# Performance work log

Measured on AMD Instinct MI355X. Metric: run time of the kernel, lower is better.

The kernel has to match this reference:

```python
import jax, jax.numpy as jnp
import numpy as np

EPS = 1e-8  # matches torch F.cosine_similarity eps


def setup_inputs() -> dict:
    key = jax.random.key(0)
    S, U, D = 2048, 10, 256  # speakers, utterances/speaker, embedding dim
    embeddings = jax.random.normal(key, (S * U, D), dtype=jnp.float32)
    labels = jnp.repeat(jnp.arange(S, dtype=jnp.int64), U)  # speaker-blocked, as the view() assumes
    return {"embeddings": embeddings, "labels": labels}


def reference(embeddings, labels):
    labels_np = np.asarray(labels)
    S = int(np.unique(labels_np).size)          # num_speakers (static)
    B, D = embeddings.shape
    U = B // S                                   # num_utterances
    E = embeddings.reshape(S, U, D)
    C = E.mean(axis=1)                           # (S, D) centroids
    En = E / jnp.maximum(jnp.linalg.norm(E, axis=-1, keepdims=True), EPS)
    Cn = C / jnp.maximum(jnp.linalg.norm(C, axis=-1, keepdims=True), EPS)
    sim = jnp.einsum('sud,kd->suk', En, Cn)      # (S, U, S) cosine similarities
    idx = jnp.arange(S)
    pos = sim[idx, :, idx]                       # (S, U) similarity to own centroid
    neg_mask = jnp.eye(S, dtype=bool)[:, None, :]  # mask out k == i
    neg = jnp.where(neg_mask, -jnp.inf, sim)
    lse = jax.nn.logsumexp(neg, axis=-1)         # (S, U)
    loss = jnp.mean(-pos + lse)
    return loss
```

## Files before the change

kernel.cpp:

```cpp
#include <hip/hip_runtime.h>
#include <math.h>

#define SS   2048
#define UU   10
#define DD   256
#define BB   (SS * UU)
#define EPSF 1e-8f

typedef __attribute__((ext_vector_type(8))) short   bf16x8;
typedef __attribute__((ext_vector_type(4))) float   floatx4;

__device__ static inline unsigned short f2bf(float f) {
    union { float f; unsigned u; } v; v.f = f;
    unsigned r = (v.u + 0x7FFFu + ((v.u >> 16) & 1u)) >> 16;
    return (unsigned short)r;
}

__device__ static inline void gl_lds16(const unsigned short* g, unsigned short* l) {
    __builtin_amdgcn_global_load_lds((const __attribute__((address_space(1))) void*)g,
                                     (__attribute__((address_space(3))) void*)l, 16, 0, 0);
}

__global__ __launch_bounds__(256) void prep_kernel(const float* __restrict__ E,
                                                   unsigned short* __restrict__ Enb,
                                                   unsigned short* __restrict__ Cnb,
                                                   float* __restrict__ sumexp,
                                                   float* __restrict__ out) {
    const int wid = threadIdx.x >> 6, lane = threadIdx.x & 63;

    if (threadIdx.x < 80) sumexp[blockIdx.x * 80 + threadIdx.x] = 0.f;
    if (blockIdx.x == 0 && threadIdx.x == 0) out[0] = 0.f;

#pragma unroll
    for (int sp2 = 0; sp2 < 2; ++sp2) {
        const int sp = blockIdx.x * 8 + wid * 2 + sp2;
        const float* rb = E + (size_t)sp * UU * DD + lane * 4;

        float4 v[UU];
#pragma unroll
        for (int u = 0; u < UU; ++u) v[u] = *(const float4*)(rb + u * DD);

        float ssq[UU];
#pragma unroll
        for (int u = 0; u < UU; ++u)
            ssq[u] = v[u].x * v[u].x + v[u].y * v[u].y + v[u].z * v[u].z + v[u].w * v[u].w;
#pragma unroll
        for (int off = 32; off; off >>= 1) {
#pragma unroll
            for (int u = 0; u < UU; ++u) ssq[u] += __shfl_xor(ssq[u], off, 64);
        }

        unsigned short* eb = Enb + (size_t)sp * UU * DD + lane * 4;
        float cx = 0.f, cy = 0.f, cz = 0.f, cw = 0.f;
#pragma unroll
        for (int u = 0; u < UU; ++u) {
            const float rinv = 1.0f / fmaxf(sqrtf(ssq[u]), EPSF);
            ushort4 o;
            o.x = f2bf(v[u].x * rinv); o.y = f2bf(v[u].y * rinv);
            o.z = f2bf(v[u].z * rinv); o.w = f2bf(v[u].w * rinv);
            *(ushort4*)(eb + u * DD) = o;
            cx += v[u].x; cy += v[u].y; cz += v[u].z; cw += v[u].w;
        }

        cx *= 0.1f; cy *= 0.1f; cz *= 0.1f; cw *= 0.1f;
        float cs = cx * cx + cy * cy + cz * cz + cw * cw;
#pragma unroll
        for (int off = 32; off; off >>= 1) cs += __shfl_xor(cs, off, 64);
        const float rinv = 1.0f / fmaxf(sqrtf(cs), EPSF);
        ushort4 oc;
        oc.x = f2bf(cx * rinv); oc.y = f2bf(cy * rinv);
        oc.z = f2bf(cz * rinv); oc.w = f2bf(cw * rinv);
        *(ushort4*)(Cnb + (size_t)sp * DD + lane * 4) = oc;
    }
}

#define BM  128
#define BN  128
#define BK  32
#define NBN 2

__device__ __forceinline__ void chunk_mfma(const unsigned short* Ab,
                                           const unsigned short* Bb,
                                           const int* aoff, const int* boff,
                                           floatx4 (&acc)[4][4]) {
    bf16x8 af[4], bfr[4];
#pragma unroll
    for (int t = 0; t < 4; ++t) af[t]  = *(const bf16x8*)(Ab + aoff[t]);
#pragma unroll
    for (int t = 0; t < 4; ++t) bfr[t] = *(const bf16x8*)(Bb + boff[t]);
#pragma unroll
    for (int mt = 0; mt < 4; ++mt)
#pragma unroll
        for (int nt = 0; nt < 4; ++nt)
            acc[mt][nt] = __builtin_amdgcn_mfma_f32_16x16x32_bf16(af[mt], bfr[nt], acc[mt][nt], 0, 0, 0);
}

__global__ __launch_bounds__(256) void gemm_lse_kernel(const unsigned short* __restrict__ Enb,
                                                       const unsigned short* __restrict__ Cnb,
                                                       float* __restrict__ posArr,
                                                       float* __restrict__ sumexp) {
    __shared__ unsigned short As[BM * BK];
    __shared__ unsigned short Bs[BN * BK];

    const int tid  = threadIdx.x;
    const int wid  = tid >> 6, lane = tid & 63;
    const int l15  = lane & 15, quad = lane >> 4;
    const int wave_m = wid >> 1, wave_n = wid & 1;

    const int swz = (blockIdx.x & 7) * 160 + (blockIdx.x >> 3);
    const int bm  = swz >> 3;
    const int bnb = (swz & 7) * NBN;
    const int row0 = bm * BM;

    const int rl = lane >> 2;
    const int gf = ((lane & 3) ^ ((rl >> 1) & 3)) * 8;
    const unsigned short* gpA[4];
    unsigned short* lp[4];
    size_t goffB[4];
#pragma unroll
    for (int i = 0; i < 4; ++i) {
        const int c = wid * 4 + i;
        if (c < 8) {
            gpA[i]  = Enb + (size_t)(row0 + c * 16 + rl) * DD + gf;
            lp[i]   = As + c * 512;
            goffB[i] = 0;
        } else {
            gpA[i]  = nullptr;
            lp[i]   = Bs + (c - 8) * 512;
            goffB[i] = (size_t)((c - 8) * 16 + rl) * DD + gf;
        }
    }

    const int fswz = (quad ^ ((l15 >> 1) & 3)) * 8;
    int aoff[4], boff[4];
#pragma unroll
    for (int t = 0; t < 4; ++t) {
        aoff[t] = (wave_m * 64 + t * 16 + l15) * BK + fswz;
        boff[t] = (wave_n * 64 + t * 16 + l15) * BK + fswz;
    }

    int lbl[4][4];
    float rs[4][4];
#pragma unroll
    for (int mt = 0; mt < 4; ++mt) {
        const int growb = row0 + wave_m * 64 + mt * 16 + quad * 4;
#pragma unroll
        for (int r = 0; r < 4; ++r) {
            lbl[mt][r] = (growb + r) / UU;
            rs[mt][r]  = 0.f;
        }
    }

    floatx4 acc[4][4];

#pragma unroll
    for (int bl = 0; bl < NBN; ++bl) {
        const int n0 = (bnb + bl) * BN;
        const unsigned short* gp[4];
#pragma unroll
        for (int i = 0; i < 4; ++i) {
            const int c = wid * 4 + i;
            gp[i] = (c < 8) ? gpA[i] : (Cnb + (size_t)n0 * DD + goffB[i]);
        }

#pragma unroll
        for (int i = 0; i < 4; ++i)
#pragma unroll
            for (int j = 0; j < 4; ++j) acc[i][j] = (floatx4){0.f, 0.f, 0.f, 0.f};

        for (int k0 = 0; k0 < DD; k0 += BK) {
            __syncthreads();
#pragma unroll
            for (int i = 0; i < 4; ++i) gl_lds16(gp[i] + k0, lp[i]);
            __syncthreads();
            chunk_mfma(As, Bs, aoff, boff, acc);
        }

#pragma unroll
        for (int mt = 0; mt < 4; ++mt) {
            const int growb = row0 + wave_m * 64 + mt * 16 + quad * 4;
#pragma unroll
            for (int nt = 0; nt < 4; ++nt) {
                const int col = n0 + wave_n * 64 + nt * 16 + l15;
#pragma unroll
                for (int r = 0; r < 4; ++r) {
                    const float sim = acc[mt][nt][r];
                    if (col == lbl[mt][r]) {
                        posArr[growb + r] = sim;
                    } else {
                        rs[mt][r] += __expf(sim);
                    }
                }
            }
        }
    }

#pragma unroll
    for (int mt = 0; mt < 4; ++mt) {
        const int growb = row0 + wave_m * 64 + mt * 16 + quad * 4;
#pragma unroll
        for (int m = 1; m < 16; m <<= 1) {
#pragma unroll
            for (int r = 0; r < 4; ++r) rs[mt][r] += __shfl_xor(rs[mt][r], m, 64);
        }
        if (l15 == 0) {
#pragma unroll
            for (int r = 0; r < 4; ++r) atomicAdd(&sumexp[growb + r], rs[mt][r]);
        }
    }
}

__global__ __launch_bounds__(256) void finalize_kernel(const float* __restrict__ posArr,
                                                       const float* __restrict__ sumexp,
                                                       float* __restrict__ out) {
    __shared__ float sred[256];
    const int tid = threadIdx.x;
    const int r = blockIdx.x * 256 + tid;
    sred[tid] = logf(sumexp[r]) - posArr[r];
    __syncthreads();
#pragma unroll
    for (int off = 128; off; off >>= 1) {
        if (tid < off) sred[tid] += sred[tid + off];
        __syncthreads();
    }
    if (tid == 0) atomicAdd(out, sred[0] * (1.0f / (float)BB));
}

extern "C" void kernel_launch(void* const* d_in, const int* in_sizes, int n_in,
                              void* d_out, int out_size, void* d_ws, size_t ws_size,
                              hipStream_t stream) {
    const float* E = (const float*)d_in[0];
    float* out = (float*)d_out;

    unsigned short* Enb = (unsigned short*)d_ws;
    unsigned short* Cnb = Enb + (size_t)BB * DD;
    float* posArr = (float*)(Cnb + (size_t)SS * DD);
    float* sumexp = posArr + BB;

    prep_kernel<<<SS / 8, 256, 0, stream>>>(E, Enb, Cnb, sumexp, out);
    gemm_lse_kernel<<<(BB / BM) * (SS / BN / NBN), 256, 0, stream>>>(Enb, Cnb, posArr, sumexp);
    finalize_kernel<<<BB / 256, 256, 0, stream>>>(posArr, sumexp, out);
}
```

Measured before the change: 114.7 us.

## Compute both N panels in one K loop to reuse the A tile

Each block now loads its A tile once per K chunk and multiplies it against two B panels held in separate LDS buffers, with two accumulator sets. Before, it looped over the two panels and reloaded A for each one. This halves the A global-to-LDS traffic and the number of barrier pairs per block. The cost is double the accumulator registers (128 floats), which risks lower occupancy or spills, plus a larger LDS footprint.

```diff
diff --git a/kernel.cpp b/kernel.cpp
--- a/kernel.cpp
+++ b/kernel.cpp
@@ -95,12 +95,37 @@
             acc[mt][nt] = __builtin_amdgcn_mfma_f32_16x16x32_bf16(af[mt], bfr[nt], acc[mt][nt], 0, 0, 0);
 }
 
+__device__ __forceinline__ void epi_panel(const floatx4 (&acc)[4][4], int n0,
+                                          int row0, int wave_m, int wave_n,
+                                          int l15, int quad,
+                                          const int (&lbl)[4][4], float (&rs)[4][4],
+                                          float* __restrict__ posArr) {
+#pragma unroll
+    for (int mt = 0; mt < 4; ++mt) {
+        const int growb = row0 + wave_m * 64 + mt * 16 + quad * 4;
+#pragma unroll
+        for (int nt = 0; nt < 4; ++nt) {
+            const int col = n0 + wave_n * 64 + nt * 16 + l15;
+#pragma unroll
+            for (int r = 0; r < 4; ++r) {
+                const float sim = acc[mt][nt][r];
+                if (col == lbl[mt][r]) {
+                    posArr[growb + r] = sim;
+                } else {
+                    rs[mt][r] += __expf(sim);
+                }
+            }
+        }
+    }
+}
+
 __global__ __launch_bounds__(256) void gemm_lse_kernel(const unsigned short* __restrict__ Enb,
                                                        const unsigned short* __restrict__ Cnb,
                                                        float* __restrict__ posArr,
                                                        float* __restrict__ sumexp) {
     __shared__ unsigned short As[BM * BK];
-    __shared__ unsigned short Bs[BN * BK];
+    __shared__ unsigned short Bs0[BN * BK];
+    __shared__ unsigned short Bs1[BN * BK];
 
     const int tid  = threadIdx.x;
     const int wid  = tid >> 6, lane = tid & 63;
@@ -111,23 +136,24 @@
     const int bm  = swz >> 3;
     const int bnb = (swz & 7) * NBN;
     const int row0 = bm * BM;
+    const int n0a  = bnb * BN, n0b = (bnb + 1) * BN;
 
     const int rl = lane >> 2;
     const int gf = ((lane & 3) ^ ((rl >> 1) & 3)) * 8;
-    const unsigned short* gpA[4];
-    unsigned short* lp[4];
-    size_t goffB[4];
-#pragma unroll
-    for (int i = 0; i < 4; ++i) {
-        const int c = wid * 4 + i;
+    const unsigned short* gp[6];
+    unsigned short* lp[6];
+#pragma unroll
+    for (int i = 0; i < 6; ++i) {
+        const int c = wid * 6 + i;
         if (c < 8) {
-            gpA[i]  = Enb + (size_t)(row0 + c * 16 + rl) * DD + gf;
-            lp[i]   = As + c * 512;
-            goffB[i] = 0;
+            gp[i] = Enb + (size_t)(row0 + c * 16 + rl) * DD + gf;
+            lp[i] = As + c * 512;
+        } else if (c < 16) {
+            gp[i] = Cnb + (size_t)(n0a + (c - 8) * 16 + rl) * DD + gf;
+            lp[i] = Bs0 + (c - 8) * 512;
         } else {
-            gpA[i]  = nullptr;
-            lp[i]   = Bs + (c - 8) * 512;
-            goffB[i] = (size_t)((c - 8) * 16 + rl) * DD + gf;
+            gp[i] = Cnb + (size_t)(n0b + (c - 16) * 16 + rl) * DD + gf;
+            lp[i] = Bs1 + (c - 16) * 512;
         }
     }
 
@@ -151,49 +177,26 @@
         }
     }
 
-    floatx4 acc[4][4];
-
-#pragma unroll
-    for (int bl = 0; bl < NBN; ++bl) {
-        const int n0 = (bnb + bl) * BN;
-        const unsigned short* gp[4];
-#pragma unroll
-        for (int i = 0; i < 4; ++i) {
-            const int c = wid * 4 + i;
-            gp[i] = (c < 8) ? gpA[i] : (Cnb + (size_t)n0 * DD + goffB[i]);
-        }
-
-#pragma unroll
-        for (int i = 0; i < 4; ++i)
-#pragma unroll
-            for (int j = 0; j < 4; ++j) acc[i][j] = (floatx4){0.f, 0.f, 0.f, 0.f};
-
-        for (int k0 = 0; k0 < DD; k0 += BK) {
-            __syncthreads();
-#pragma unroll
-            for (int i = 0; i < 4; ++i) gl_lds16(gp[i] + k0, lp[i]);
-            __syncthreads();
-            chunk_mfma(As, Bs, aoff, boff, acc);
-        }
-
-#pragma unroll
-        for (int mt = 0; mt < 4; ++mt) {
-            const int growb = row0 + wave_m * 64 + mt * 16 + quad * 4;
-#pragma unroll
-            for (int nt = 0; nt < 4; ++nt) {
-                const int col = n0 + wave_n * 64 + nt * 16 + l15;
-#pragma unroll
-                for (int r = 0; r < 4; ++r) {
-                    const float sim = acc[mt][nt][r];
-                    if (col == lbl[mt][r]) {
-                        posArr[growb + r] = sim;
-                    } else {
-                        rs[mt][r] += __expf(sim);
-                    }
-                }
-            }
-        }
-    }
+    floatx4 acc0[4][4], acc1[4][4];
+#pragma unroll
+    for (int i = 0; i < 4; ++i)
+#pragma unroll
+        for (int j = 0; j < 4; ++j) {
+            acc0[i][j] = (floatx4){0.f, 0.f, 0.f, 0.f};
+            acc1[i][j] = (floatx4){0.f, 0.f, 0.f, 0.f};
+        }
+
+    for (int k0 = 0; k0 < DD; k0 += BK) {
+        __syncthreads();
+#pragma unroll
+        for (int i = 0; i < 6; ++i) gl_lds16(gp[i] + k0, lp[i]);
+        __syncthreads();
+        chunk_mfma(As, Bs0, aoff, boff, acc0);
+        chunk_mfma(As, Bs1, aoff, boff, acc1);
+    }
+
+    epi_panel(acc0, n0a, row0, wave_m, wave_n, l15, quad, lbl, rs, posArr);
+    epi_panel(acc1, n0b, row0, wave_m, wave_n, l15, quad, lbl, rs, posArr);
 
 #pragma unroll
     for (int mt = 0; mt < 4; ++mt) {
```

New measurement: 151.7 us. 1.32x slower.

## Drop per-block N-loop, double K chunk per barrier, launch one tile per block

Applied to the files above, without the earlier changes.

Each block now computes a single 128x128 output tile instead of two sequential column tiles, which doubles the grid to 2560 blocks. The K loop now stages 64 elements per barrier pair as two 32-wide halves in LDS, halving the number of syncthreads in the GEMM. This adds parallelism and cuts barrier overhead, but reloads the A tile once per column tile, doubles LDS use per block and issues more sumexp atomics.

```diff
diff --git a/kernel.cpp b/kernel.cpp
--- a/kernel.cpp
+++ b/kernel.cpp
@@ -76,8 +76,8 @@
 
 #define BM  128
 #define BN  128
-#define BK  32
-#define NBN 2
+#define BK  64
+#define CHK 32
 
 __device__ __forceinline__ void chunk_mfma(const unsigned short* Ab,
                                            const unsigned short* Bb,
@@ -99,35 +99,35 @@
                                                        const unsigned short* __restrict__ Cnb,
                                                        float* __restrict__ posArr,
                                                        float* __restrict__ sumexp) {
-    __shared__ unsigned short As[BM * BK];
-    __shared__ unsigned short Bs[BN * BK];
+    __shared__ unsigned short As[2 * BM * CHK];
+    __shared__ unsigned short Bs[2 * BN * CHK];
 
     const int tid  = threadIdx.x;
     const int wid  = tid >> 6, lane = tid & 63;
     const int l15  = lane & 15, quad = lane >> 4;
     const int wave_m = wid >> 1, wave_n = wid & 1;
 
-    const int swz = (blockIdx.x & 7) * 160 + (blockIdx.x >> 3);
-    const int bm  = swz >> 3;
-    const int bnb = (swz & 7) * NBN;
-    const int row0 = bm * BM;
+    const int swz = (blockIdx.x & 7) * 320 + (blockIdx.x >> 3);
+    const int bn = swz & 15;
+    const int bm = swz >> 4;
+    const int row0 = bm * BM, n0 = bn * BN;
 
     const int rl = lane >> 2;
     const int gf = ((lane & 3) ^ ((rl >> 1) & 3)) * 8;
-    const unsigned short* gpA[4];
-    unsigned short* lp[4];
-    size_t goffB[4];
-#pragma unroll
-    for (int i = 0; i < 4; ++i) {
-        const int c = wid * 4 + i;
-        if (c < 8) {
-            gpA[i]  = Enb + (size_t)(row0 + c * 16 + rl) * DD + gf;
-            lp[i]   = As + c * 512;
-            goffB[i] = 0;
+    const unsigned short* gp[8];
+    unsigned short* lp[8];
+#pragma unroll
+    for (int i = 0; i < 8; ++i) {
+        const int c   = wid * 8 + i;
+        const int op  = c >> 4;
+        const int kh  = (c >> 3) & 1;
+        const int sub = c & 7;
+        if (op == 0) {
+            gp[i] = Enb + (size_t)(row0 + sub * 16 + rl) * DD + kh * CHK + gf;
+            lp[i] = As + kh * (BM * CHK) + sub * 512;
         } else {
-            gpA[i]  = nullptr;
-            lp[i]   = Bs + (c - 8) * 512;
-            goffB[i] = (size_t)((c - 8) * 16 + rl) * DD + gf;
+            gp[i] = Cnb + (size_t)(n0 + sub * 16 + rl) * DD + kh * CHK + gf;
+            lp[i] = Bs + kh * (BN * CHK) + sub * 512;
         }
     }
 
@@ -135,77 +135,51 @@
     int aoff[4], boff[4];
 #pragma unroll
     for (int t = 0; t < 4; ++t) {
-        aoff[t] = (wave_m * 64 + t * 16 + l15) * BK + fswz;
-        boff[t] = (wave_n * 64 + t * 16 + l15) * BK + fswz;
-    }
-
-    int lbl[4][4];
-    float rs[4][4];
+        aoff[t] = (wave_m * 64 + t * 16 + l15) * CHK + fswz;
+        boff[t] = (wave_n * 64 + t * 16 + l15) * CHK + fswz;
+    }
+
+    floatx4 acc[4][4];
+#pragma unroll
+    for (int i = 0; i < 4; ++i)
+#pragma unroll
+        for (int j = 0; j < 4; ++j) acc[i][j] = (floatx4){0.f, 0.f, 0.f, 0.f};
+
+    for (int k0 = 0; k0 < DD; k0 += BK) {
+        __syncthreads();
+#pragma unroll
+        for (int i = 0; i < 8; ++i) gl_lds16(gp[i] + k0, lp[i]);
+        __syncthreads();
+        chunk_mfma(As, Bs, aoff, boff, acc);
+        chunk_mfma(As + BM * CHK, Bs + BN * CHK, aoff, boff, acc);
+    }
+
 #pragma unroll
     for (int mt = 0; mt < 4; ++mt) {
+        float rs[4] = {0.f, 0.f, 0.f, 0.f};
         const int growb = row0 + wave_m * 64 + mt * 16 + quad * 4;
 #pragma unroll
-        for (int r = 0; r < 4; ++r) {
-            lbl[mt][r] = (growb + r) / UU;
-            rs[mt][r]  = 0.f;
-        }
-    }
-
-    floatx4 acc[4][4];
-
-#pragma unroll
-    for (int bl = 0; bl < NBN; ++bl) {
-        const int n0 = (bnb + bl) * BN;
-        const unsigned short* gp[4];
-#pragma unroll
-        for (int i = 0; i < 4; ++i) {
-            const int c = wid * 4 + i;
-            gp[i] = (c < 8) ? gpA[i] : (Cnb + (size_t)n0 * DD + goffB[i]);
-        }
-
-#pragma unroll
-        for (int i = 0; i < 4; ++i)
-#pragma unroll
-            for (int j = 0; j < 4; ++j) acc[i][j] = (floatx4){0.f, 0.f, 0.f, 0.f};
-
-        for (int k0 = 0; k0 < DD; k0 += BK) {
-            __syncthreads();
-#pragma unroll
-            for (int i = 0; i < 4; ++i) gl_lds16(gp[i] + k0, lp[i]);
-            __syncthreads();
-            chunk_mfma(As, Bs, aoff, boff, acc);
-        }
-
-#pragma unroll
-        for (int mt = 0; mt < 4; ++mt) {
-            const int growb = row0 + wave_m * 64 + mt * 16 + quad * 4;
-#pragma unroll
-            for (int nt = 0; nt < 4; ++nt) {
-                const int col = n0 + wave_n * 64 + nt * 16 + l15;
-#pragma unroll
-                for (int r = 0; r < 4; ++r) {
-                    const float sim = acc[mt][nt][r];
-                    if (col == lbl[mt][r]) {
-                        posArr[growb + r] = sim;
-                    } else {
-                        rs[mt][r] += __expf(sim);
-                    }
+        for (int nt = 0; nt < 4; ++nt) {
+            const int col = n0 + wave_n * 64 + nt * 16 + l15;
+#pragma unroll
+            for (int r = 0; r < 4; ++r) {
+                const int grow = growb + r;
+                const float sim = acc[mt][nt][r];
+                if (col == grow / UU) {
+                    posArr[grow] = sim;
+                } else {
+                    rs[r] += __expf(sim);
                 }
             }
         }
-    }
-
-#pragma unroll
-    for (int mt = 0; mt < 4; ++mt) {
-        const int growb = row0 + wave_m * 64 + mt * 16 + quad * 4;
 #pragma unroll
         for (int m = 1; m < 16; m <<= 1) {
 #pragma unroll
-            for (int r = 0; r < 4; ++r) rs[mt][r] += __shfl_xor(rs[mt][r], m, 64);
+            for (int r = 0; r < 4; ++r) rs[r] += __shfl_xor(rs[r], m, 64);
         }
         if (l15 == 0) {
 #pragma unroll
-            for (int r = 0; r < 4; ++r) atomicAdd(&sumexp[growb + r], rs[mt][r]);
+            for (int r = 0; r < 4; ++r) atomicAdd(&sumexp[growb + r], rs[r]);
         }
     }
 }
@@ -238,6 +212,6 @@
     float* sumexp = posArr + BB;
 
     prep_kernel<<<SS / 8, 256, 0, stream>>>(E, Enb, Cnb, sumexp, out);
-    gemm_lse_kernel<<<(BB / BM) * (SS / BN / NBN), 256, 0, stream>>>(Enb, Cnb, posArr, sumexp);
+    gemm_lse_kernel<<<(BB / BM) * (SS / BN), 256, 0, stream>>>(Enb, Cnb, posArr, sumexp);
     finalize_kernel<<<BB / 256, 256, 0, stream>>>(posArr, sumexp, out);
 }
```

Result: slower. 120.2 us (+4.8%).
